# Kernel optimization log

Hardware: AMD Instinct MI355X
Metric: run time of the kernel (lower is better)

The kernel has to match this reference:

```python
import jax, jax.numpy as jnp
import numpy as np

B, N, F_DIM, HID, HEADS = 4, 1024, 512, 64, 8  # feature_dim == HID*HEADS required by the module's += broadcast


def setup_inputs() -> dict:
    key = jax.random.key(0)
    ks = jax.random.split(key, 16)
    s = 0.05
    return {
        'node_features_a': jax.random.normal(ks[0], (B, N, F_DIM), dtype=jnp.float32),
        'node_features_b': jax.random.normal(ks[1], (B, N, F_DIM), dtype=jnp.float32),
        'A_intra_a': jax.random.uniform(ks[2], (B, N, N), dtype=jnp.float32),
        'A_intra_b': jax.random.uniform(ks[3], (B, N, N), dtype=jnp.float32),
        'A_inter': jax.random.uniform(ks[4], (B, N, N), dtype=jnp.float32),
        # stacked per-head Linear weights (torch ModuleList F1/F2/F3), [H, F, K]
        'W1': jax.random.normal(ks[5], (HEADS, F_DIM, HID), dtype=jnp.float32) * s,
        'b1': jnp.zeros((HEADS, HID), jnp.float32),
        'W2': jax.random.normal(ks[6], (HEADS, F_DIM, HID), dtype=jnp.float32) * s,
        'b2': jnp.zeros((HEADS, HID), jnp.float32),
        'W3': jax.random.normal(ks[7], (HEADS, F_DIM, HID), dtype=jnp.float32) * s,
        'b3': jnp.zeros((HEADS, HID), jnp.float32),
        'W_intra_a': jax.random.normal(ks[8], (HID, HID), dtype=jnp.float32) * s,
        'W_intra_b': jax.random.normal(ks[9], (HID, HID), dtype=jnp.float32) * s,
        'W_inter': jax.random.normal(ks[10], (HID, HID), dtype=jnp.float32) * s,
        'W_out': jax.random.normal(ks[11], (F_DIM, HID * HEADS), dtype=jnp.float32) * s,  # torch Linear weight [out,in]
        'b_out': jnp.zeros((F_DIM,), jnp.float32),
        'b_output': jnp.zeros((F_DIM,), jnp.float32),
    }


def _aggregate(src, tgt, adj, ew, W1, b1, W2, b2, W3, b3, W_out, b_out, b_output):
    # per-head projections, batched over heads instead of a Python loop
    F1u = jnp.einsum('bnf,hfk->bhnk', src, W1) + b1[:, None, :]
    F2v = jnp.einsum('bmf,hfk->bhmk', tgt, W2) + b2[:, None, :]
    F3u = jnp.einsum('bnf,hfk->bhnk', src, W3) + b3[:, None, :]
    # attention_scores = F1_u @ (edge_weight @ F2_v^T)  -> [B,H,N,N]
    scores = jnp.einsum('bhnk,kl,bhml->bhnm', F1u, ew, F2v)
    # multiplicative adjacency mask, then softmax over last dim
    attn = jax.nn.softmax(scores * adj[:, None, :, :], axis=-1)
    msgs = jnp.einsum('bhnm,bhmk->bhnk', attn, F3u)
    b_, h_, n_, k_ = msgs.shape
    concat = msgs.transpose(0, 2, 1, 3).reshape(b_, n_, h_ * k_)  # cat heads on last dim
    return jax.nn.relu(concat @ W_out.T + b_out) + b_output


def reference(node_features_a, node_features_b, A_intra_a, A_intra_b, A_inter,
              W1, b1, W2, b2, W3, b3, W_intra_a, W_intra_b, W_inter,
              W_out, b_out, b_output):
    p = (W1, b1, W2, b2, W3, b3)
    o = (W_out, b_out, b_output)
    ua = _aggregate(node_features_a, node_features_a, A_intra_a, W_intra_a, *p, *o)
    ub = _aggregate(node_features_b, node_features_b, A_intra_b, W_intra_b, *p, *o)
    ia = _aggregate(node_features_a, node_features_b, A_inter, W_inter, *p, *o)
    ib = _aggregate(node_features_b, node_features_a, jnp.swapaxes(A_inter, 1, 2), W_inter, *p, *o)
    return (ua + ia, ub + ib)
```

## Files before the change

### kernel.cpp

```cpp
#include <hip/hip_runtime.h>
#include <hip/hip_bf16.h>

#define BB 4
#define NN 1024
#define FF 512
#define HH 8
#define KK 64
#define PSZ ((size_t)BB * HH * NN * KK)

#define XAOFF 0u
#define XBOFF 2097152u
#define WTOFF 4194304u
#define WOOFF (WTOFF + 786432u)
#define PBOFF (WOOFF + 262144u)
#define MSOFF (PBOFF + 6u * 2097152u)
#define ADOFF (MSOFF + 4u * 2097152u)
#define ADSZ  4194304u

#define LOG2E 1.4426950408889634f
#define SHIFT2 34.624683f

typedef unsigned short u16;
typedef __attribute__((ext_vector_type(8))) short bf16x8;
typedef __attribute__((ext_vector_type(4))) short bf16x4;
typedef __attribute__((ext_vector_type(4))) float f32x4;
typedef __attribute__((ext_vector_type(8))) unsigned short ushort8;
typedef __attribute__((ext_vector_type(4))) unsigned short ushort4v;

#if defined(__has_builtin)
#if __has_builtin(__builtin_amdgcn_mfma_f32_16x16x16bf16_1k)
#define HAVE_MFMA16 1
#endif
#if __has_builtin(__builtin_amdgcn_global_load_lds)
#define HAVE_GLL 1
#endif
#endif
#ifndef HAVE_MFMA16
#define HAVE_MFMA16 0
#endif
#ifndef HAVE_GLL
#define HAVE_GLL 0
#endif

#if HAVE_GLL
#define GSTR 64
#else
#define GSTR 72
#endif

__device__ __forceinline__ u16 f2b(float x) {
    union { float f; unsigned u; } v; v.f = x;
    unsigned r = v.u + 0x7FFF + ((v.u >> 16) & 1);
    return (u16)(r >> 16);
}
__device__ __forceinline__ float b2f(u16 x) {
    union { unsigned u; float f; } v; v.u = ((unsigned)x) << 16;
    return v.f;
}

__global__ __launch_bounds__(256) void prep_kernel(
    const float* __restrict__ Xa, const float* __restrict__ Xb,
    const float* __restrict__ Wout,
    const float* __restrict__ Aia, const float* __restrict__ Aib,
    const float* __restrict__ Ain,
    const float* __restrict__ W1, const float* __restrict__ W2,
    const float* __restrict__ W3,
    u16* __restrict__ ws)
{
    __shared__ float T[64][65];
    const int bid = blockIdx.x;
    const int t = threadIdx.x;

    if (bid < 192) {
        const int j  = bid / 64;
        const int rem = bid & 63;
        const int h  = rem >> 3;
        const int f0 = (rem & 7) * 64;
        const float* Wj = j == 0 ? W1 : (j == 1 ? W2 : W3);
        const int tr = t >> 2, tc = (t & 3) * 16;
        const float* src = Wj + (size_t)h * FF * KK + (size_t)(f0 + tr) * KK + tc;
        #pragma unroll
        for (int jj = 0; jj < 4; ++jj) {
            float4 v = *(const float4*)(src + 4 * jj);
            T[tr][tc + 4 * jj + 0] = v.x;
            T[tr][tc + 4 * jj + 1] = v.y;
            T[tr][tc + 4 * jj + 2] = v.z;
            T[tr][tc + 4 * jj + 3] = v.w;
        }
        __syncthreads();
        ushort8 w0, w1;
        #pragma unroll
        for (int jj = 0; jj < 8; ++jj) {
            w0[jj] = f2b(T[tc + jj][tr]);
            w1[jj] = f2b(T[tc + 8 + jj][tr]);
        }
        u16* d = ws + WTOFF + (unsigned)j * 262144u + (unsigned)(h * 64 + tr) * 512u + f0 + tc;
        *(ushort8*)&d[0] = w0;
        *(ushort8*)&d[8] = w1;
        return;
    }

    const int NFLAT4 = (2097152 + 2097152 + 262144) / 4;
    const int NADJ4  = 3 * 1048576;
    const int total  = NFLAT4 + NADJ4;
    const int nb = gridDim.x - 192;
    for (int idx = (bid - 192) * 256 + t; idx < total; idx += nb * 256) {
        if (idx < NFLAT4) {
            int e = idx * 4;
            const float* src; u16* dst;
            if (e < 2097152)      { src = Xa + e;             dst = ws + XAOFF + e; }
            else if (e < 4194304) { src = Xb + (e - 2097152); dst = ws + XBOFF + (e - 2097152); }
            else                  { src = Wout + (e - 4194304); dst = ws + WOOFF + (e - 4194304); }
            float4 v = *(const float4*)src;
            ushort4v w;
            w[0] = f2b(v.x); w[1] = f2b(v.y); w[2] = f2b(v.z); w[3] = f2b(v.w);
            *(ushort4v*)dst = w;
        } else {
            int r = idx - NFLAT4;
            int z = r >> 20;
            int rem = r & 1048575;
            const float* src = (z == 0 ? Aia : (z == 1 ? Aib : Ain)) + (size_t)rem * 4;
            float4 v = *(const float4*)src;
            ushort4v w;
            w[0] = f2b(v.x * LOG2E); w[1] = f2b(v.y * LOG2E);
            w[2] = f2b(v.z * LOG2E); w[3] = f2b(v.w * LOG2E);
            *(ushort4v*)(ws + ADOFF + (size_t)z * ADSZ + (size_t)rem * 4) = w;
        }
    }
}

__global__ __launch_bounds__(256) void tr_kernel(const float* __restrict__ A, u16* __restrict__ dst)
{
    const int b = blockIdx.z;
    const int r0 = blockIdx.y * 64, c0 = blockIdx.x * 64;
    __shared__ float T[64][65];
    const int t = threadIdx.x;
    const int tr = t >> 2, tc = (t & 3) * 16;
    const float* src = A + ((size_t)b * NN + r0 + tr) * NN + c0 + tc;
    #pragma unroll
    for (int j = 0; j < 4; ++j) {
        float4 v = *(const float4*)(src + 4 * j);
        T[tr][tc + 4 * j + 0] = v.x;
        T[tr][tc + 4 * j + 1] = v.y;
        T[tr][tc + 4 * j + 2] = v.z;
        T[tr][tc + 4 * j + 3] = v.w;
    }
    __syncthreads();
    ushort8 w0, w1;
    #pragma unroll
    for (int j = 0; j < 8; ++j) {
        w0[j] = f2b(T[tc + j][tr] * LOG2E);
        w1[j] = f2b(T[tc + 8 + j][tr] * LOG2E);
    }
    u16* d = dst + ((size_t)b * NN + c0 + tr) * NN + r0 + tc;
    *(ushort8*)&d[0] = w0;
    *(ushort8*)&d[8] = w1;
}

__global__ __launch_bounds__(256) void proj_kernel(
    const float* __restrict__ b1v, const float* __restrict__ b2v,
    const float* __restrict__ b3v,
    u16* __restrict__ ws)
{
    const int z  = blockIdx.z;
    const int src = z / 3, pj = z % 3;
    const u16* X  = ws + (src ? XBOFF : XAOFF);
    const u16* Wt = ws + WTOFF + (unsigned)pj * 262144u;
    const float* bias = pj == 0 ? b1v : (pj == 1 ? b2v : b3v);
    u16* P = ws + PBOFF + (size_t)z * PSZ;

    const int rb = blockIdx.y * 128;
    const int cb = blockIdx.x * 128;
    const int t  = threadIdx.x;
    const int lane = t & 63, wave = t >> 6;
    const int lg = lane >> 4, li = lane & 15;
    const int wr = wave >> 1, wc = wave & 1;

    __shared__ u16 As[128 * GSTR];
    __shared__ u16 Bs[128 * GSTR];

    f32x4 acc[4][4];
    #pragma unroll
    for (int m = 0; m < 4; ++m)
        #pragma unroll
        for (int n = 0; n < 4; ++n) acc[m][n] = (f32x4){0.f, 0.f, 0.f, 0.f};

#if !HAVE_GLL
    const int srow = t >> 1, sf0 = (t & 1) * 32;
#endif

    for (int fb = 0; fb < FF; fb += 64) {
        __syncthreads();
#if HAVE_GLL
        {
            const int gr = wave * 32 + (lane >> 3);
            const int gc = (lane & 7) * 8;
            #pragma unroll
            for (int i = 0; i < 4; ++i) {
                __builtin_amdgcn_global_load_lds(
                    (const unsigned int*)&X[(size_t)(rb + gr + 8 * i) * FF + fb + gc],
                    (unsigned int*)&As[(wave * 32 + 8 * i) * GSTR], 16, 0, 0);
                __builtin_amdgcn_global_load_lds(
                    (const unsigned int*)&Wt[(size_t)(cb + gr + 8 * i) * FF + fb + gc],
                    (unsigned int*)&Bs[(wave * 32 + 8 * i) * GSTR], 16, 0, 0);
            }
        }
#else
        #pragma unroll
        for (int s = 0; s < 4; ++s) {
            *(ushort8*)&As[srow * GSTR + sf0 + 8 * s] =
                *(const ushort8*)&X[(size_t)(rb + srow) * FF + fb + sf0 + 8 * s];
            *(ushort8*)&Bs[srow * GSTR + sf0 + 8 * s] =
                *(const ushort8*)&Wt[(size_t)(cb + srow) * FF + fb + sf0 + 8 * s];
        }
#endif
        __syncthreads();

        bf16x8 af[4][2], bf[4][2];
        #pragma unroll
        for (int m = 0; m < 4; ++m) {
            af[m][0] = *(const bf16x8*)&As[(wr * 64 + m * 16 + li) * GSTR + 8 * lg];
            af[m][1] = *(const bf16x8*)&As[(wr * 64 + m * 16 + li) * GSTR + 8 * lg + 32];
        }
        #pragma unroll
        for (int n = 0; n < 4; ++n) {
            bf[n][0] = *(const bf16x8*)&Bs[(wc * 64 + n * 16 + li) * GSTR + 8 * lg];
            bf[n][1] = *(const bf16x8*)&Bs[(wc * 64 + n * 16 + li) * GSTR + 8 * lg + 32];
        }
        #pragma unroll
        for (int m = 0; m < 4; ++m)
            #pragma unroll
            for (int n = 0; n < 4; ++n) {
                acc[m][n] = __builtin_amdgcn_mfma_f32_16x16x32_bf16(af[m][0], bf[n][0], acc[m][n], 0, 0, 0);
                acc[m][n] = __builtin_amdgcn_mfma_f32_16x16x32_bf16(af[m][1], bf[n][1], acc[m][n], 0, 0, 0);
            }
    }

    if (pj != 2) {
        #pragma unroll
        for (int m = 0; m < 4; ++m)
            #pragma unroll
            for (int n = 0; n < 4; ++n)
                #pragma unroll
                for (int r = 0; r < 4; ++r) {
                    int row = rb + wr * 64 + m * 16 + 4 * lg + r;
                    int col = cb + wc * 64 + n * 16 + li;
                    int b_ = row >> 10, n_ = row & 1023;
                    int h = col >> 6, k = col & 63;
                    P[((size_t)(b_ * HH + h) * NN + n_) * KK + k] = f2b(acc[m][n][r] + bias[col]);
                }
    } else {
        #pragma unroll
        for (int m = 0; m < 4; ++m)
            #pragma unroll
            for (int n = 0; n < 4; ++n) {
                int col = cb + wc * 64 + n * 16 + li;
                int h = col >> 6, k = col & 63;
                int row0 = rb + wr * 64 + m * 16 + 4 * lg;
                int b_ = row0 >> 10, n0 = row0 & 1023;
                float bsv = bias[col];
                ushort4v w;
                #pragma unroll
                for (int r = 0; r < 4; ++r) w[r] = f2b(acc[m][n][r] + bsv);
                *(ushort4v*)&P[((size_t)(b_ * HH + h) * KK + k) * NN + n0] = w;
            }
    }
}

__global__ __launch_bounds__(256, 4) void attn_kernel(
    const u16* __restrict__ Pbase,
    const float* __restrict__ Wia, const float* __restrict__ Wib, const float* __restrict__ Win,
    const u16* __restrict__ AD, const u16* __restrict__ AinT,
    u16* __restrict__ msgs)
{
    const int flat = blockIdx.x;
    const int lf   = (flat & 7) * 128 + (flat >> 3);
    const int qb   = (lf & 7) * 128;
    const int bh   = (lf >> 3) & 31;
    const int agg  = lf >> 8;
    const int b = bh >> 3, h = bh & 7;
    const int t = threadIdx.x;
    const int lane = t & 63, wave = t >> 6;
    const int lg = lane >> 4, li = lane & 15;

    const u16 *Qp, *Kp, *Vp, *adj; const float* ew;
    switch (agg) {
      case 0: Qp = Pbase;         ew = Wia; Kp = Pbase + 1*PSZ; Vp = Pbase + 2*PSZ; adj = AD;          break;
      case 1: Qp = Pbase + 3*PSZ; ew = Wib; Kp = Pbase + 4*PSZ; Vp = Pbase + 5*PSZ; adj = AD + 1*ADSZ; break;
      case 2: Qp = Pbase;         ew = Win; Kp = Pbase + 4*PSZ; Vp = Pbase + 2*PSZ; adj = AD + 2*ADSZ; break;
      default:Qp = Pbase + 3*PSZ; ew = Win; Kp = Pbase + 1*PSZ; Vp = Pbase + 5*PSZ; adj = AinT;        break;
    }
    const size_t bhoff = (size_t)(b * HH + h) * NN * KK;
    const u16* Qbh  = Qp + bhoff;
    const u16* Kbh  = Kp + bhoff;
    const u16* Vbh  = Vp + bhoff;
    const u16* adjb = adj + (size_t)b * NN * NN;

    __shared__ u16 Qa[128 * 72];
    __shared__ u16 Kt[64 * 72];
    __shared__ u16 Vt[64 * 72];

    const int sr  = t >> 2;
    const int sc  = (t & 3) * 16;
    const int sr2 = t >> 1;
    const int sc2 = (t & 1) * 32;

    #pragma unroll
    for (int j = 0; j < 16; ++j)
        Vt[(sc + j) * 72 + sr] = f2b(ew[sr * 64 + sc + j]);

    #pragma unroll
    for (int p = 0; p < 2; ++p) {
        __syncthreads();
        {
            const ushort8* src = (const ushort8*)&Qbh[(size_t)(qb + p * 64 + sr) * KK + sc];
            *(ushort8*)&Kt[sr * 72 + sc]     = src[0];
            *(ushort8*)&Kt[sr * 72 + sc + 8] = src[1];
        }
        __syncthreads();
        bf16x8 a0 = *(const bf16x8*)&Kt[(wave * 16 + li) * 72 + 8 * lg];
        bf16x8 a1 = *(const bf16x8*)&Kt[(wave * 16 + li) * 72 + 8 * lg + 32];
        #pragma unroll
        for (int t_ = 0; t_ < 4; ++t_) {
            bf16x8 b0 = *(const bf16x8*)&Vt[(li + 16 * t_) * 72 + 8 * lg];
            bf16x8 b1 = *(const bf16x8*)&Vt[(li + 16 * t_) * 72 + 8 * lg + 32];
            f32x4 q = {0.f, 0.f, 0.f, 0.f};
            q = __builtin_amdgcn_mfma_f32_16x16x32_bf16(a0, b0, q, 0, 0, 0);
            q = __builtin_amdgcn_mfma_f32_16x16x32_bf16(a1, b1, q, 0, 0, 0);
            #pragma unroll
            for (int r = 0; r < 4; ++r)
                Qa[(p * 64 + wave * 16 + 4 * lg + r) * 72 + li + 16 * t_] = f2b(q[r]);
        }
    }
    __syncthreads();
    bf16x8 qB[2][2];
    #pragma unroll
    for (int u = 0; u < 2; ++u)
        #pragma unroll
        for (int c = 0; c < 2; ++c)
            qB[u][c] = *(const bf16x8*)&Qa[(wave * 32 + u * 16 + li) * 72 + 32 * c + 8 * lg];
    __syncthreads();

    f32x4 oacc[2][4];
    #pragma unroll
    for (int u = 0; u < 2; ++u)
        #pragma unroll
        for (int f_ = 0; f_ < 4; ++f_) oacc[u][f_] = (f32x4){0.f, 0.f, 0.f, 0.f};
    float lsum[2] = {0.f, 0.f};

    for (int mt = 0; mt < 16; ++mt) {
        const int mb = mt * 64;
        {
            const ushort8* ks = (const ushort8*)&Kbh[(size_t)(mb + sr) * KK + sc];
            *(ushort8*)&Kt[sr * 72 + sc]     = ks[0];
            *(ushort8*)&Kt[sr * 72 + sc + 8] = ks[1];
            const ushort8* vs = (const ushort8*)&Vbh[(size_t)sr * NN + mb + sc];
            *(ushort8*)&Vt[sr * 72 + sc]     = vs[0];
            *(ushort8*)&Vt[sr * 72 + sc + 8] = vs[1];
            const u16* ap = &adjb[(size_t)(qb + sr2) * NN + mb + sc2];
            #pragma unroll
            for (int s = 0; s < 4; ++s)
                *(ushort8*)&Qa[sr2 * 72 + sc2 + 8 * s] = *(const ushort8*)&ap[8 * s];
        }
        __syncthreads();

        ushort4v adv[2][4];
        #pragma unroll
        for (int u = 0; u < 2; ++u)
            #pragma unroll
            for (int t_ = 0; t_ < 4; ++t_)
                adv[u][t_] = *(const ushort4v*)&Qa[(wave * 32 + u * 16 + li) * 72 + 16 * t_ + 4 * lg];

#if HAVE_MFMA16
        bf16x4 pa[2][4];
#endif
        #pragma unroll
        for (int t_ = 0; t_ < 4; ++t_) {
            bf16x8 kb0 = *(const bf16x8*)&Kt[(li + 16 * t_) * 72 + 8 * lg];
            bf16x8 kb1 = *(const bf16x8*)&Kt[(li + 16 * t_) * 72 + 8 * lg + 32];
            #pragma unroll
            for (int u = 0; u < 2; ++u) {
                f32x4 s = {0.f, 0.f, 0.f, 0.f};
                __builtin_amdgcn_s_setprio(1);
                s = __builtin_amdgcn_mfma_f32_16x16x32_bf16(kb0, qB[u][0], s, 0, 0, 0);
                s = __builtin_amdgcn_mfma_f32_16x16x32_bf16(kb1, qB[u][1], s, 0, 0, 0);
                __builtin_amdgcn_s_setprio(0);
                float p0 = __builtin_amdgcn_exp2f(fmaf(s[0], b2f(adv[u][t_][0]), -SHIFT2));
                float p1 = __builtin_amdgcn_exp2f(fmaf(s[1], b2f(adv[u][t_][1]), -SHIFT2));
                float p2 = __builtin_amdgcn_exp2f(fmaf(s[2], b2f(adv[u][t_][2]), -SHIFT2));
                float p3 = __builtin_amdgcn_exp2f(fmaf(s[3], b2f(adv[u][t_][3]), -SHIFT2));
                lsum[u] += (p0 + p1) + (p2 + p3);
                unsigned w0, w1;
                asm("v_cvt_pk_bf16_f32 %0, %1, %2" : "=v"(w0) : "v"(p0), "v"(p1));
                asm("v_cvt_pk_bf16_f32 %0, %1, %2" : "=v"(w1) : "v"(p2), "v"(p3));
#if HAVE_MFMA16
                union { uint2 u2; bf16x4 v; } pk;
                pk.u2.x = w0; pk.u2.y = w1;
                pa[u][t_] = pk.v;
#else
                uint2 pd; pd.x = w0; pd.y = w1;
                *(uint2*)&Qa[(wave * 32 + u * 16 + li) * 72 + 16 * t_ + 4 * lg] = pd;
#endif
            }
        }

#if HAVE_MFMA16
        __builtin_amdgcn_s_setprio(1);
        #pragma unroll
        for (int f_ = 0; f_ < 4; ++f_) {
            #pragma unroll
            for (int t_ = 0; t_ < 4; ++t_) {
                bf16x4 vb = *(const bf16x4*)&Vt[(li + 16 * f_) * 72 + 16 * t_ + 4 * lg];
                #pragma unroll
                for (int u = 0; u < 2; ++u)
                    oacc[u][f_] = __builtin_amdgcn_mfma_f32_16x16x16bf16_1k(pa[u][t_], vb, oacc[u][f_], 0, 0, 0);
            }
        }
        __builtin_amdgcn_s_setprio(0);
#else
        {
            bf16x8 pA[2][2];
            #pragma unroll
            for (int u = 0; u < 2; ++u) {
                pA[u][0] = *(const bf16x8*)&Qa[(wave * 32 + u * 16 + li) * 72 + 8 * lg];
                pA[u][1] = *(const bf16x8*)&Qa[(wave * 32 + u * 16 + li) * 72 + 8 * lg + 32];
            }
            #pragma unroll
            for (int f_ = 0; f_ < 4; ++f_) {
                bf16x8 vb0 = *(const bf16x8*)&Vt[(li + 16 * f_) * 72 + 8 * lg];
                bf16x8 vb1 = *(const bf16x8*)&Vt[(li + 16 * f_) * 72 + 8 * lg + 32];
                #pragma unroll
                for (int u = 0; u < 2; ++u) {
                    oacc[u][f_] = __builtin_amdgcn_mfma_f32_16x16x32_bf16(pA[u][0], vb0, oacc[u][f_], 0, 0, 0);
                    oacc[u][f_] = __builtin_amdgcn_mfma_f32_16x16x32_bf16(pA[u][1], vb1, oacc[u][f_], 0, 0, 0);
                }
            }
        }
#endif
        __syncthreads();
    }

    #pragma unroll
    for (int u = 0; u < 2; ++u) {
        lsum[u] += __shfl_xor(lsum[u], 16);
        lsum[u] += __shfl_xor(lsum[u], 32);
    }
    #pragma unroll
    for (int u = 0; u < 2; ++u)
        #pragma unroll
        for (int r = 0; r < 4; ++r) {
            float inv = 1.f / __shfl(lsum[u], 4 * lg + r);
            int row = qb + wave * 32 + u * 16 + 4 * lg + r;
            u16* dst = msgs + (size_t)agg * PSZ + ((size_t)b * NN + row) * (HH * KK) + h * KK;
            #pragma unroll
            for (int f_ = 0; f_ < 4; ++f_)
                dst[li + 16 * f_] = f2b(oacc[u][f_][r] * inv);
        }
}

__global__ __launch_bounds__(256) void out_kernel(
    const u16* __restrict__ ws,
    const float* __restrict__ bo, const float* __restrict__ bo2,
    float* __restrict__ out)
{
    const int z  = blockIdx.z;
    const u16* M1 = ws + MSOFF + (size_t)z * PSZ;
    const u16* M2 = ws + MSOFF + (size_t)(2 + z) * PSZ;
    const u16* Wb = ws + WOOFF;
    const int rb = blockIdx.y * 64;
    const int cb = blockIdx.x * 128;
    const int t  = threadIdx.x;
    const int lane = t & 63, wave = t >> 6;
    const int lg = lane >> 4, li = lane & 15;
    const int wr = wave >> 1, wc = wave & 1;

    __shared__ u16 A1s[64 * GSTR];
    __shared__ u16 A2s[64 * GSTR];
    __shared__ u16 Bs[128 * GSTR];

    f32x4 acc1[2][4], acc2[2][4];
    #pragma unroll
    for (int m = 0; m < 2; ++m)
        #pragma unroll
        for (int n = 0; n < 4; ++n) {
            acc1[m][n] = (f32x4){0.f, 0.f, 0.f, 0.f};
            acc2[m][n] = (f32x4){0.f, 0.f, 0.f, 0.f};
        }

    for (int fb = 0; fb < FF; fb += 64) {
        __syncthreads();
#if HAVE_GLL
        {
            const int lr = lane >> 3;
            const int gc = (lane & 7) * 8;
            #pragma unroll
            for (int i = 0; i < 2; ++i) {
                __builtin_amdgcn_global_load_lds(
                    (const unsigned int*)&M1[(size_t)(rb + wave * 16 + 8 * i + lr) * FF + fb + gc],
                    (unsigned int*)&A1s[(wave * 16 + 8 * i) * GSTR], 16, 0, 0);
                __builtin_amdgcn_global_load_lds(
                    (const unsigned int*)&M2[(size_t)(rb + wave * 16 + 8 * i + lr) * FF + fb + gc],
                    (unsigned int*)&A2s[(wave * 16 + 8 * i) * GSTR], 16, 0, 0);
            }
            #pragma unroll
            for (int i = 0; i < 4; ++i) {
                __builtin_amdgcn_global_load_lds(
                    (const unsigned int*)&Wb[(size_t)(cb + wave * 32 + 8 * i + lr) * FF + fb + gc],
                    (unsigned int*)&Bs[(wave * 32 + 8 * i) * GSTR], 16, 0, 0);
            }
        }
#else
        {
            int ar = t >> 2, ac = (t & 3) * 16;
            *(ushort8*)&A1s[ar * GSTR + ac]     = *(const ushort8*)&M1[(size_t)(rb + ar) * FF + fb + ac];
            *(ushort8*)&A1s[ar * GSTR + ac + 8] = *(const ushort8*)&M1[(size_t)(rb + ar) * FF + fb + ac + 8];
            *(ushort8*)&A2s[ar * GSTR + ac]     = *(const ushort8*)&M2[(size_t)(rb + ar) * FF + fb + ac];
            *(ushort8*)&A2s[ar * GSTR + ac + 8] = *(const ushort8*)&M2[(size_t)(rb + ar) * FF + fb + ac + 8];
            int br = t >> 1, bc = (t & 1) * 32;
            #pragma unroll
            for (int s = 0; s < 4; ++s)
                *(ushort8*)&Bs[br * GSTR + bc + 8 * s] =
                    *(const ushort8*)&Wb[(size_t)(cb + br) * FF + fb + bc + 8 * s];
        }
#endif
        __syncthreads();

        #pragma unroll
        for (int m = 0; m < 2; ++m) {
            bf16x8 a10 = *(const bf16x8*)&A1s[(wr * 32 + m * 16 + li) * GSTR + 8 * lg];
            bf16x8 a11 = *(const bf16x8*)&A1s[(wr * 32 + m * 16 + li) * GSTR + 8 * lg + 32];
            bf16x8 a20 = *(const bf16x8*)&A2s[(wr * 32 + m * 16 + li) * GSTR + 8 * lg];
            bf16x8 a21 = *(const bf16x8*)&A2s[(wr * 32 + m * 16 + li) * GSTR + 8 * lg + 32];
            #pragma unroll
            for (int n = 0; n < 4; ++n) {
                bf16x8 b0 = *(const bf16x8*)&Bs[(wc * 64 + n * 16 + li) * GSTR + 8 * lg];
                bf16x8 b1 = *(const bf16x8*)&Bs[(wc * 64 + n * 16 + li) * GSTR + 8 * lg + 32];
                acc1[m][n] = __builtin_amdgcn_mfma_f32_16x16x32_bf16(a10, b0, acc1[m][n], 0, 0, 0);
                acc1[m][n] = __builtin_amdgcn_mfma_f32_16x16x32_bf16(a11, b1, acc1[m][n], 0, 0, 0);
                acc2[m][n] = __builtin_amdgcn_mfma_f32_16x16x32_bf16(a20, b0, acc2[m][n], 0, 0, 0);
                acc2[m][n] = __builtin_amdgcn_mfma_f32_16x16x32_bf16(a21, b1, acc2[m][n], 0, 0, 0);
            }
        }
    }

    #pragma unroll
    for (int m = 0; m < 2; ++m)
        #pragma unroll
        for (int n = 0; n < 4; ++n)
            #pragma unroll
            for (int r = 0; r < 4; ++r) {
                int row = rb + wr * 32 + m * 16 + 4 * lg + r;
                int col = cb + wc * 64 + n * 16 + li;
                float v1 = fmaxf(acc1[m][n][r] + bo[col], 0.f);
                float v2 = fmaxf(acc2[m][n][r] + bo[col], 0.f);
                out[(size_t)z * (BB * NN * FF) + (size_t)row * FF + col] = v1 + v2 + 2.f * bo2[col];
            }
}

extern "C" void kernel_launch(void* const* d_in, const int* in_sizes, int n_in,
                              void* d_out, int out_size, void* d_ws, size_t ws_size,
                              hipStream_t stream) {
    const float* nfa  = (const float*)d_in[0];
    const float* nfb  = (const float*)d_in[1];
    const float* Aia  = (const float*)d_in[2];
    const float* Aib  = (const float*)d_in[3];
    const float* Ain  = (const float*)d_in[4];
    const float* W1   = (const float*)d_in[5];
    const float* b1   = (const float*)d_in[6];
    const float* W2   = (const float*)d_in[7];
    const float* b2   = (const float*)d_in[8];
    const float* W3   = (const float*)d_in[9];
    const float* b3   = (const float*)d_in[10];
    const float* Wia  = (const float*)d_in[11];
    const float* Wib  = (const float*)d_in[12];
    const float* Win  = (const float*)d_in[13];
    const float* Wout = (const float*)d_in[14];
    const float* bo   = (const float*)d_in[15];
    const float* bo2  = (const float*)d_in[16];

    u16* ws = (u16*)d_ws;
    float* out = (float*)d_out;

    prep_kernel<<<4096, 256, 0, stream>>>(nfa, nfb, Wout, Aia, Aib, Ain, W1, W2, W3, ws);
    proj_kernel<<<dim3(4, 32, 6), 256, 0, stream>>>(b1, b2, b3, ws);
    tr_kernel<<<dim3(16, 16, 4), 256, 0, stream>>>(Ain, ws + XAOFF);
    attn_kernel<<<1024, 256, 0, stream>>>(ws + PBOFF, Wia, Wib, Win, ws + ADOFF, ws + XAOFF, ws + MSOFF);
    out_kernel<<<dim3(4, 64, 2), 256, 0, stream>>>(ws, bo, bo2, out);
}
```

Before: 135.0 us.

## Double-buffer K/V tiles via global_load_lds with swizzled LDS and register-prefetched adjacency

Rewrites the attention main loop to double-buffer the K and V tiles in LDS. Tiles are loaded asynchronously with global_load_lds into an XOR-swizzled layout, so the next tile's loads overlap the current tile's MFMA and exp work. Adjacency values are now prefetched straight from global memory into registers one tile ahead instead of being staged through LDS. This replaces the per-iteration load-then-sync pattern with explicit vmcnt waits and barriers, which adds complexity and relies on exact wait counts for correctness.

```diff
diff --git a/kernel.cpp b/kernel.cpp
--- a/kernel.cpp
+++ b/kernel.cpp
@@ -296,40 +296,39 @@
     const u16* Vbh  = Vp + bhoff;
     const u16* adjb = adj + (size_t)b * NN * NN;
 
-    __shared__ u16 Qa[128 * 72];
-    __shared__ u16 Kt[64 * 72];
-    __shared__ u16 Vt[64 * 72];
+    __shared__ __align__(16) char smem[36864];
+    u16* preQ = (u16*)smem;
+    u16* preF = (u16*)(smem + 18432);
+    u16* preE = (u16*)(smem + 27648);
 
     const int sr  = t >> 2;
     const int sc  = (t & 3) * 16;
-    const int sr2 = t >> 1;
-    const int sc2 = (t & 1) * 32;
 
     #pragma unroll
     for (int j = 0; j < 16; ++j)
-        Vt[(sc + j) * 72 + sr] = f2b(ew[sr * 64 + sc + j]);
+        preE[(sc + j) * 72 + sr] = f2b(ew[sr * 64 + sc + j]);
 
     #pragma unroll
     for (int p = 0; p < 2; ++p) {
         __syncthreads();
         {
             const ushort8* src = (const ushort8*)&Qbh[(size_t)(qb + p * 64 + sr) * KK + sc];
-            *(ushort8*)&Kt[sr * 72 + sc]     = src[0];
-            *(ushort8*)&Kt[sr * 72 + sc + 8] = src[1];
-        }
-        __syncthreads();
-        bf16x8 a0 = *(const bf16x8*)&Kt[(wave * 16 + li) * 72 + 8 * lg];
-        bf16x8 a1 = *(const bf16x8*)&Kt[(wave * 16 + li) * 72 + 8 * lg + 32];
+            *(ushort8*)&preF[sr * 72 + sc]     = src[0];
+            *(ushort8*)&preF[sr * 72 + sc + 8] = src[1];
+        }
+        __syncthreads();
+        bf16x8 a0 = *(const bf16x8*)&preF[(wave * 16 + li) * 72 + 8 * lg];
+        bf16x8 a1 = *(const bf16x8*)&preF[(wave * 16 + li) * 72 + 8 * lg + 32];
         #pragma unroll
         for (int t_ = 0; t_ < 4; ++t_) {
-            bf16x8 b0 = *(const bf16x8*)&Vt[(li + 16 * t_) * 72 + 8 * lg];
-            bf16x8 b1 = *(const bf16x8*)&Vt[(li + 16 * t_) * 72 + 8 * lg + 32];
+            bf16x8 b0 = *(const bf16x8*)&preE[(li + 16 * t_) * 72 + 8 * lg];
+            bf16x8 b1 = *(const bf16x8*)&preE[(li + 16 * t_) * 72 + 8 * lg + 32];
             f32x4 q = {0.f, 0.f, 0.f, 0.f};
             q = __builtin_amdgcn_mfma_f32_16x16x32_bf16(a0, b0, q, 0, 0, 0);
             q = __builtin_amdgcn_mfma_f32_16x16x32_bf16(a1, b1, q, 0, 0, 0);
             #pragma unroll
             for (int r = 0; r < 4; ++r)
-                Qa[(p * 64 + wave * 16 + 4 * lg + r) * 72 + li + 16 * t_] = f2b(q[r]);
+                preQ[(p * 64 + wave * 16 + 4 * lg + r) * 72 + li + 16 * t_] = f2b(q[r]);
         }
     }
     __syncthreads();
@@ -338,7 +337,7 @@
     for (int u = 0; u < 2; ++u)
         #pragma unroll
         for (int c = 0; c < 2; ++c)
-            qB[u][c] = *(const bf16x8*)&Qa[(wave * 32 + u * 16 + li) * 72 + 32 * c + 8 * lg];
+            qB[u][c] = *(const bf16x8*)&preQ[(wave * 32 + u * 16 + li) * 72 + 32 * c + 8 * lg];
     __syncthreads();
 
     f32x4 oacc[2][4];
@@ -348,6 +347,117 @@
         for (int f_ = 0; f_ < 4; ++f_) oacc[u][f_] = (f32x4){0.f, 0.f, 0.f, 0.f};
     float lsum[2] = {0.f, 0.f};
 
+#if HAVE_GLL && HAVE_MFMA16
+#define SWZB(ROW, OFF) (((ROW) << 7) + ((OFF) ^ (((ROW) & 7) << 4)))
+
+#define STAGE(MB2, BUF)                                                         \
+    {                                                                           \
+        _Pragma("unroll")                                                       \
+        for (int i_ = 0; i_ < 2; ++i_) {                                        \
+            int row_ = i_ * 32 + (t >> 3);                                      \
+            int c16_ = (t & 7) ^ (row_ & 7);                                    \
+            __builtin_amdgcn_global_load_lds(                                   \
+                (const unsigned int*)&Kbh[(size_t)((MB2) + row_) * KK + c16_ * 8], \
+                (unsigned int*)(smem + (BUF) * 8192 + i_ * 4096 + wave * 1024), \
+                16, 0, 0);                                                      \
+        }                                                                       \
+        _Pragma("unroll")                                                       \
+        for (int i_ = 0; i_ < 2; ++i_) {                                        \
+            int row_ = i_ * 32 + (t >> 3);                                      \
+            int c16_ = (t & 7) ^ (row_ & 7);                                    \
+            __builtin_amdgcn_global_load_lds(                                   \
+                (const unsigned int*)&Vbh[(size_t)row_ * NN + (MB2) + c16_ * 8],\
+                (unsigned int*)(smem + 16384 + (BUF) * 8192 + i_ * 4096 + wave * 1024), \
+                16, 0, 0);                                                      \
+        }                                                                       \
+    }
+
+#define LOADADV(DST, MB2)                                                       \
+    {                                                                           \
+        _Pragma("unroll")                                                       \
+        for (int u_ = 0; u_ < 2; ++u_)                                          \
+            _Pragma("unroll")                                                   \
+            for (int t2_ = 0; t2_ < 4; ++t2_)                                   \
+                DST[u_][t2_] = *(const ushort4v*)&adjb[                         \
+                    (size_t)(qb + wave * 32 + u_ * 16 + li) * NN + (MB2) + 16 * t2_ + 4 * lg]; \
+    }
+
+#define ATTN_ITER(MT, CUR, ADVC, ADVN)                                          \
+    {                                                                           \
+        __builtin_amdgcn_s_barrier();                      \
+        __builtin_amdgcn_sched_barrier(0);                                      \
+        if ((MT) < 15) {                                                        \
+            STAGE(((MT) + 1) * 64, (CUR) ^ 1);                                  \
+            asm volatile("s_waitcnt vmcnt(12)" ::: "memory");                   \
+        } else {                                                                \
+            asm volatile("s_waitcnt vmcnt(8)" ::: "memory");                    \
+        }                                                                       \
+        __builtin_amdgcn_s_barrier();                     \
+        __builtin_amdgcn_sched_barrier(0);                                      \
+        if ((MT) < 15) { LOADADV(ADVN, ((MT) + 1) * 64); }                      \
+        const char* Kc = smem + (CUR) * 8192;                                   \
+        const char* Vc = smem + 16384 + (CUR) * 8192;                           \
+        bf16x4 pa[2][4];                                                        \
+        _Pragma("unroll")                                                       \
+        for (int t_ = 0; t_ < 4; ++t_) {                                        \
+            int krow = li + 16 * t_;                                            \
+            bf16x8 kb0 = *(const bf16x8*)(Kc + SWZB(krow, 16 * lg));            \
+            bf16x8 kb1 = *(const bf16x8*)(Kc + SWZB(krow, 16 * lg + 64));       \
+            _Pragma("unroll")                                                   \
+            for (int u = 0; u < 2; ++u) {                                       \
+                f32x4 s = {0.f, 0.f, 0.f, 0.f};                                 \
+                __builtin_amdgcn_s_setprio(1);                                  \
+                s = __builtin_amdgcn_mfma_f32_16x16x32_bf16(kb0, qB[u][0], s, 0, 0, 0); \
+                s = __builtin_amdgcn_mfma_f32_16x16x32_bf16(kb1, qB[u][1], s, 0, 0, 0); \
+                __builtin_amdgcn_s_setprio(0);                                  \
+                float p0 = __builtin_amdgcn_exp2f(fmaf(s[0], b2f(ADVC[u][t_][0]), -SHIFT2)); \
+                float p1 = __builtin_amdgcn_exp2f(fmaf(s[1], b2f(ADVC[u][t_][1]), -SHIFT2)); \
+                float p2 = __builtin_amdgcn_exp2f(fmaf(s[2], b2f(ADVC[u][t_][2]), -SHIFT2)); \
+                float p3 = __builtin_amdgcn_exp2f(fmaf(s[3], b2f(ADVC[u][t_][3]), -SHIFT2)); \
+                lsum[u] += (p0 + p1) + (p2 + p3);                               \
+                unsigned w0, w1;                                                \
+                asm("v_cvt_pk_bf16_f32 %0, %1, %2" : "=v"(w0) : "v"(p0), "v"(p1)); \
+                asm("v_cvt_pk_bf16_f32 %0, %1, %2" : "=v"(w1) : "v"(p2), "v"(p3)); \
+                union { uint2 u2; bf16x4 v; } pk;                               \
+                pk.u2.x = w0; pk.u2.y = w1;                                     \
+                pa[u][t_] = pk.v;                                               \
+            }                                                                   \
+        }                                                                       \
+        __builtin_amdgcn_s_setprio(1);                                          \
+        _Pragma("unroll")                                                       \
+        for (int f_ = 0; f_ < 4; ++f_) {                                        \
+            int vrow = li + 16 * f_;                                            \
+            _Pragma("unroll")                                                   \
+            for (int t_ = 0; t_ < 4; ++t_) {                                    \
+                bf16x4 vb = *(const bf16x4*)(Vc + SWZB(vrow, 32 * t_ + 8 * lg));\
+                oacc[0][f_] = __builtin_amdgcn_mfma_f32_16x16x16bf16_1k(pa[0][t_], vb, oacc[0][f_], 0, 0, 0); \
+                oacc[1][f_] = __builtin_amdgcn_mfma_f32_16x16x16bf16_1k(pa[1][t_], vb, oacc[1][f_], 0, 0, 0); \
+            }                                                                   \
+        }                                                                       \
+        __builtin_amdgcn_s_setprio(0);                                          \
+    }
+
+    ushort4v advA[2][4], advB[2][4];
+    STAGE(0, 0);
+    LOADADV(advA, 0);
+
+    #pragma unroll 1
+    for (int mt2 = 0; mt2 < 8; ++mt2) {
+        const int mtE = 2 * mt2;
+        ATTN_ITER(mtE, 0, advA, advB);
+        const int mtO = 2 * mt2 + 1;
+        ATTN_ITER(mtO, 1, advB, advA);
+    }
+#undef ATTN_ITER
+#undef LOADADV
+#undef STAGE
+#undef SWZB
+#else
+    u16* Qa = preQ;
+    u16* Kt = preF;
+    u16* Vt = preE;
+    const int sr2 = t >> 1;
+    const int sc2 = (t & 1) * 32;
     for (int mt = 0; mt < 16; ++mt) {
         const int mb = mt * 64;
         {
@@ -371,9 +481,6 @@
             for (int t_ = 0; t_ < 4; ++t_)
                 adv[u][t_] = *(const ushort4v*)&Qa[(wave * 32 + u * 16 + li) * 72 + 16 * t_ + 4 * lg];
 
-#if HAVE_MFMA16
-        bf16x4 pa[2][4];
-#endif
         #pragma unroll
         for (int t_ = 0; t_ < 4; ++t_) {
             bf16x8 kb0 = *(const bf16x8*)&Kt[(li + 16 * t_) * 72 + 8 * lg];
@@ -381,10 +488,8 @@
             #pragma unroll
             for (int u = 0; u < 2; ++u) {
                 f32x4 s = {0.f, 0.f, 0.f, 0.f};
-                __builtin_amdgcn_s_setprio(1);
                 s = __builtin_amdgcn_mfma_f32_16x16x32_bf16(kb0, qB[u][0], s, 0, 0, 0);
                 s = __builtin_amdgcn_mfma_f32_16x16x32_bf16(kb1, qB[u][1], s, 0, 0, 0);
-                __builtin_amdgcn_s_setprio(0);
                 float p0 = __builtin_amdgcn_exp2f(fmaf(s[0], b2f(adv[u][t_][0]), -SHIFT2));
                 float p1 = __builtin_amdgcn_exp2f(fmaf(s[1], b2f(adv[u][t_][1]), -SHIFT2));
                 float p2 = __builtin_amdgcn_exp2f(fmaf(s[2], b2f(adv[u][t_][2]), -SHIFT2));
@@ -393,31 +498,10 @@
                 unsigned w0, w1;
                 asm("v_cvt_pk_bf16_f32 %0, %1, %2" : "=v"(w0) : "v"(p0), "v"(p1));
                 asm("v_cvt_pk_bf16_f32 %0, %1, %2" : "=v"(w1) : "v"(p2), "v"(p3));
-#if HAVE_MFMA16
-                union { uint2 u2; bf16x4 v; } pk;
-                pk.u2.x = w0; pk.u2.y = w1;
-                pa[u][t_] = pk.v;
-#else
                 uint2 pd; pd.x = w0; pd.y = w1;
                 *(uint2*)&Qa[(wave * 32 + u * 16 + li) * 72 + 16 * t_ + 4 * lg] = pd;
-#endif
-            }
-        }
-
-#if HAVE_MFMA16
-        __builtin_amdgcn_s_setprio(1);
-        #pragma unroll
-        for (int f_ = 0; f_ < 4; ++f_) {
-            #pragma unroll
-            for (int t_ = 0; t_ < 4; ++t_) {
-                bf16x4 vb = *(const bf16x4*)&Vt[(li + 16 * f_) * 72 + 16 * t_ + 4 * lg];
-                #pragma unroll
-                for (int u = 0; u < 2; ++u)
-                    oacc[u][f_] = __builtin_amdgcn_mfma_f32_16x16x16bf16_1k(pa[u][t_], vb, oacc[u][f_], 0, 0, 0);
-            }
-        }
-        __builtin_amdgcn_s_setprio(0);
-#else
+            }
+        }
         {
             bf16x8 pA[2][2];
             #pragma unroll
@@ -436,9 +520,9 @@
                 }
             }
         }
-#endif
-        __syncthreads();
-    }
+        __syncthreads();
+    }
+#endif
 
     #pragma unroll
     for (int u = 0; u < 2; ++u) {
```

Result: slower. 250.6 us (+85.6%).

## Read K, V and adjacency directly from global memory, dropping LDS staging and barriers

Applied to the files above, without the earlier changes.

On the MFMA16 path, the attention loop stops staging K, V and adjacency tiles through shared memory. Each lane now loads its MFMA operands straight from global memory, which removes both per-iteration __syncthreads and the LDS write/read round trips. The cost is that the four waves each fetch the same K and V tiles, relying on L1/L2 hits. The adjacency loads also become narrow, strided 8-byte gathers.

```diff
diff --git a/kernel.cpp b/kernel.cpp
--- a/kernel.cpp
+++ b/kernel.cpp
@@ -302,8 +302,6 @@
 
     const int sr  = t >> 2;
     const int sc  = (t & 3) * 16;
-    const int sr2 = t >> 1;
-    const int sc2 = (t & 1) * 32;
 
     #pragma unroll
     for (int j = 0; j < 16; ++j)
@@ -339,7 +337,6 @@
         #pragma unroll
         for (int c = 0; c < 2; ++c)
             qB[u][c] = *(const bf16x8*)&Qa[(wave * 32 + u * 16 + li) * 72 + 32 * c + 8 * lg];
-    __syncthreads();
 
     f32x4 oacc[2][4];
     #pragma unroll
@@ -348,36 +345,25 @@
         for (int f_ = 0; f_ < 4; ++f_) oacc[u][f_] = (f32x4){0.f, 0.f, 0.f, 0.f};
     float lsum[2] = {0.f, 0.f};
 
+#if HAVE_MFMA16
+    const int q0 = qb + wave * 32 + li;
+    #pragma unroll 1
     for (int mt = 0; mt < 16; ++mt) {
         const int mb = mt * 64;
-        {
-            const ushort8* ks = (const ushort8*)&Kbh[(size_t)(mb + sr) * KK + sc];
-            *(ushort8*)&Kt[sr * 72 + sc]     = ks[0];
-            *(ushort8*)&Kt[sr * 72 + sc + 8] = ks[1];
-            const ushort8* vs = (const ushort8*)&Vbh[(size_t)sr * NN + mb + sc];
-            *(ushort8*)&Vt[sr * 72 + sc]     = vs[0];
-            *(ushort8*)&Vt[sr * 72 + sc + 8] = vs[1];
-            const u16* ap = &adjb[(size_t)(qb + sr2) * NN + mb + sc2];
-            #pragma unroll
-            for (int s = 0; s < 4; ++s)
-                *(ushort8*)&Qa[sr2 * 72 + sc2 + 8 * s] = *(const ushort8*)&ap[8 * s];
-        }
-        __syncthreads();
 
         ushort4v adv[2][4];
         #pragma unroll
         for (int u = 0; u < 2; ++u)
             #pragma unroll
             for (int t_ = 0; t_ < 4; ++t_)
-                adv[u][t_] = *(const ushort4v*)&Qa[(wave * 32 + u * 16 + li) * 72 + 16 * t_ + 4 * lg];
-
-#if HAVE_MFMA16
+                adv[u][t_] = *(const ushort4v*)&adjb[(size_t)(q0 + u * 16) * NN + mb + 16 * t_ + 4 * lg];
+
         bf16x4 pa[2][4];
-#endif
         #pragma unroll
         for (int t_ = 0; t_ < 4; ++t_) {
-            bf16x8 kb0 = *(const bf16x8*)&Kt[(li + 16 * t_) * 72 + 8 * lg];
-            bf16x8 kb1 = *(const bf16x8*)&Kt[(li + 16 * t_) * 72 + 8 * lg + 32];
+            const u16* krow = &Kbh[(size_t)(mb + li + 16 * t_) * KK + 8 * lg];
+            bf16x8 kb0 = *(const bf16x8*)&krow[0];
+            bf16x8 kb1 = *(const bf16x8*)&krow[32];
             #pragma unroll
             for (int u = 0; u < 2; ++u) {
                 f32x4 s = {0.f, 0.f, 0.f, 0.f};
@@ -393,31 +379,73 @@
                 unsigned w0, w1;
                 asm("v_cvt_pk_bf16_f32 %0, %1, %2" : "=v"(w0) : "v"(p0), "v"(p1));
                 asm("v_cvt_pk_bf16_f32 %0, %1, %2" : "=v"(w1) : "v"(p2), "v"(p3));
-#if HAVE_MFMA16
                 union { uint2 u2; bf16x4 v; } pk;
                 pk.u2.x = w0; pk.u2.y = w1;
                 pa[u][t_] = pk.v;
+            }
+        }
+
+        __builtin_amdgcn_s_setprio(1);
+        #pragma unroll
+        for (int f_ = 0; f_ < 4; ++f_) {
+            const u16* vrow = &Vbh[(size_t)(li + 16 * f_) * NN + mb + 4 * lg];
+            #pragma unroll
+            for (int t_ = 0; t_ < 4; ++t_) {
+                bf16x4 vb = *(const bf16x4*)&vrow[16 * t_];
+                oacc[0][f_] = __builtin_amdgcn_mfma_f32_16x16x16bf16_1k(pa[0][t_], vb, oacc[0][f_], 0, 0, 0);
+                oacc[1][f_] = __builtin_amdgcn_mfma_f32_16x16x16bf16_1k(pa[1][t_], vb, oacc[1][f_], 0, 0, 0);
+            }
+        }
+        __builtin_amdgcn_s_setprio(0);
+    }
 #else
+    __syncthreads();
+    const int sr2 = t >> 1;
+    const int sc2 = (t & 1) * 32;
+    for (int mt = 0; mt < 16; ++mt) {
+        const int mb = mt * 64;
+        {
+            const ushort8* ks = (const ushort8*)&Kbh[(size_t)(mb + sr) * KK + sc];
+            *(ushort8*)&Kt[sr * 72 + sc]     = ks[0];
+            *(ushort8*)&Kt[sr * 72 + sc + 8] = ks[1];
+            const ushort8* vs = (const ushort8*)&Vbh[(size_t)sr * NN + mb + sc];
+            *(ushort8*)&Vt[sr * 72 + sc]     = vs[0];
+            *(ushort8*)&Vt[sr * 72 + sc + 8] = vs[1];
+            const u16* ap = &adjb[(size_t)(qb + sr2) * NN + mb + sc2];
+            #pragma unroll
+            for (int s = 0; s < 4; ++s)
+                *(ushort8*)&Qa[sr2 * 72 + sc2 + 8 * s] = *(const ushort8*)&ap[8 * s];
+        }
+        __syncthreads();
+
+        ushort4v adv[2][4];
+        #pragma unroll
+        for (int u = 0; u < 2; ++u)
+            #pragma unroll
+            for (int t_ = 0; t_ < 4; ++t_)
+                adv[u][t_] = *(const ushort4v*)&Qa[(wave * 32 + u * 16 + li) * 72 + 16 * t_ + 4 * lg];
+
+        #pragma unroll
+        for (int t_ = 0; t_ < 4; ++t_) {
+            bf16x8 kb0 = *(const bf16x8*)&Kt[(li + 16 * t_) * 72 + 8 * lg];
+            bf16x8 kb1 = *(const bf16x8*)&Kt[(li + 16 * t_) * 72 + 8 * lg + 32];
+            #pragma unroll
+            for (int u = 0; u < 2; ++u) {
+                f32x4 s = {0.f, 0.f, 0.f, 0.f};
+                s = __builtin_amdgcn_mfma_f32_16x16x32_bf16(kb0, qB[u][0], s, 0, 0, 0);
+                s = __builtin_amdgcn_mfma_f32_16x16x32_bf16(kb1, qB[u][1], s, 0, 0, 0);
+                float p0 = __builtin_amdgcn_exp2f(fmaf(s[0], b2f(adv[u][t_][0]), -SHIFT2));
+                float p1 = __builtin_amdgcn_exp2f(fmaf(s[1], b2f(adv[u][t_][1]), -SHIFT2));
+                float p2 = __builtin_amdgcn_exp2f(fmaf(s[2], b2f(adv[u][t_][2]), -SHIFT2));
+                float p3 = __builtin_amdgcn_exp2f(fmaf(s[3], b2f(adv[u][t_][3]), -SHIFT2));
+                lsum[u] += (p0 + p1) + (p2 + p3);
+                unsigned w0, w1;
+                asm("v_cvt_pk_bf16_f32 %0, %1, %2" : "=v"(w0) : "v"(p0), "v"(p1));
+                asm("v_cvt_pk_bf16_f32 %0, %1, %2" : "=v"(w1) : "v"(p2), "v"(p3));
                 uint2 pd; pd.x = w0; pd.y = w1;
                 *(uint2*)&Qa[(wave * 32 + u * 16 + li) * 72 + 16 * t_ + 4 * lg] = pd;
-#endif
-            }
-        }
-
-#if HAVE_MFMA16
-        __builtin_amdgcn_s_setprio(1);
-        #pragma unroll
-        for (int f_ = 0; f_ < 4; ++f_) {
-            #pragma unroll
-            for (int t_ = 0; t_ < 4; ++t_) {
-                bf16x4 vb = *(const bf16x4*)&Vt[(li + 16 * f_) * 72 + 16 * t_ + 4 * lg];
-                #pragma unroll
-                for (int u = 0; u < 2; ++u)
-                    oacc[u][f_] = __builtin_amdgcn_mfma_f32_16x16x16bf16_1k(pa[u][t_], vb, oacc[u][f_], 0, 0, 0);
-            }
-        }
-        __builtin_amdgcn_s_setprio(0);
-#else
+            }
+        }
         {
             bf16x8 pA[2][2];
             #pragma unroll
@@ -436,9 +464,9 @@
                 }
             }
         }
-#endif
-        __syncthreads();
-    }
+        __syncthreads();
+    }
+#endif
 
     #pragma unroll
     for (int u = 0; u < 2; ++u) {
```

New measurement: 302.0 us. 2.24x slower.
